# Kernel optimization log

Measured on AMD Instinct MI355X. Metric: run time of the kernel, lower is better.

The kernel has to match this reference:

```python
import jax, jax.numpy as jnp
import numpy as np

HIDDEN = 2560
HEADS = 32
HEAD_DIM = HIDDEN // HEADS  # 80
ROT = HEAD_DIM // 2         # partial_rotary_factor=0.5 -> 40
B = 2
S = 2048
T = B * S
THETA = 10000.0


def setup_inputs() -> dict:
    key = jax.random.key(0)
    k0, k1, k2, k3, k4 = jax.random.split(key, 5)
    hidden_states = jax.random.normal(k0, (T, HIDDEN), jnp.float32)
    w_qkv = jax.random.normal(k1, (3 * HIDDEN, HIDDEN), jnp.float32) * 0.02
    b_qkv = jax.random.normal(k2, (3 * HIDDEN,), jnp.float32) * 0.02
    w_o = jax.random.normal(k3, (HIDDEN, HIDDEN), jnp.float32) * 0.02
    b_o = jax.random.normal(k4, (HIDDEN,), jnp.float32) * 0.02
    # rotary tables for positions 0..S-1 per sequence, rotary_dim=ROT
    pos = jnp.tile(jnp.arange(S, dtype=jnp.float32), B)  # [T]
    inv_freq = 1.0 / (THETA ** (jnp.arange(0, ROT, 2, dtype=jnp.float32) / ROT))  # [ROT//2]
    freqs = pos[:, None] * inv_freq[None, :]  # [T, ROT//2]
    return {
        "hidden_states": hidden_states,
        "w_qkv": w_qkv,
        "b_qkv": b_qkv,
        "w_o": w_o,
        "b_o": b_o,
        "cos": jnp.cos(freqs),
        "sin": jnp.sin(freqs),
        "batch": B,
    }


def _apply_rope(x, cos, sin):
    # x: [T, H, D]; rotate first ROT dims NeoX-style (rotate_half)
    half = ROT // 2
    x1 = x[..., :half]
    x2 = x[..., half:ROT]
    c = cos[:, None, :]
    s = sin[:, None, :]
    return jnp.concatenate([x1 * c - x2 * s, x1 * s + x2 * c, x[..., ROT:]], axis=-1)


def reference(hidden_states, w_qkv, b_qkv, w_o, b_o, cos, sin, batch):
    t, hdim = hidden_states.shape
    seq = t // batch
    # fused QKV projection (with bias)
    qkv = hidden_states @ w_qkv.T + b_qkv  # [T, 3*HIDDEN]
    q, k, v = jnp.split(qkv, 3, axis=1)
    q = _apply_rope(q.reshape(t, HEADS, HEAD_DIM), cos, sin)
    k = _apply_rope(k.reshape(t, HEADS, HEAD_DIM), cos, sin)
    v = v.reshape(t, HEADS, HEAD_DIM)
    # prefill causal attention per sequence
    qb = q.reshape(batch, seq, HEADS, HEAD_DIM)
    kb = k.reshape(batch, seq, HEADS, HEAD_DIM)
    vb = v.reshape(batch, seq, HEADS, HEAD_DIM)
    scale = 1.0 / jnp.sqrt(jnp.float32(HEAD_DIM))
    scores = jnp.einsum("bqhd,bkhd->bhqk", qb, kb) * scale  # [B,H,S,S]
    causal = jnp.tril(jnp.ones((seq, seq), dtype=bool))
    scores = jnp.where(causal[None, None], scores, jnp.finfo(scores.dtype).min)
    attn = jax.nn.softmax(scores, axis=-1)
    out = jnp.einsum("bhqk,bkhd->bqhd", attn, vb).reshape(t, HIDDEN)
    return out @ w_o.T + b_o
```

## Files before the change

kernel.cpp:

```cpp
#include <hip/hip_runtime.h>
#include <hip/hip_bf16.h>

#define HID   2560
#define NH    32
#define HD    80
#define SEQ   2048
#define TTOT  4096
#define QKVN  7680

typedef float  f32x4  __attribute__((ext_vector_type(4)));
typedef short  short8 __attribute__((ext_vector_type(8)));
typedef __bf16 bf16x8 __attribute__((ext_vector_type(8)));
typedef __hip_bfloat16 bf16;

__device__ __forceinline__ float bf2f(bf16 h) { return __bfloat162float(h); }
__device__ __forceinline__ bf16  f2bf(float f) { return __float2bfloat16(f); }

__device__ __forceinline__ f32x4 mfma16(short8 a, short8 b, f32x4 c) {
  return __builtin_amdgcn_mfma_f32_16x16x32_bf16(
      __builtin_bit_cast(bf16x8, a), __builtin_bit_cast(bf16x8, b), c, 0, 0, 0);
}

typedef __attribute__((address_space(1))) const unsigned int as1_uint;
typedef __attribute__((address_space(3))) unsigned int       as3_uint;
__device__ __forceinline__ void gld16(const void* g, void* l) {
  __builtin_amdgcn_global_load_lds((as1_uint*)g, (as3_uint*)l, 16, 0, 0);
}

__global__ void detect_kernel(const unsigned short* __restrict__ hid, int* flag) {
  const int tid = threadIdx.x;
  const unsigned short u = hid[2 * (tid * 997)];
  const int e = (u >> 7) & 0xFF;
  const int sane = (u == 0 || (e >= 0x60 && e <= 0x8A)) ? 1 : 0;
  __shared__ int cnt;
  if (tid == 0) cnt = 0;
  __syncthreads();
  atomicAdd(&cnt, sane);
  __syncthreads();
  if (tid == 0) *flag = (cnt < 160) ? 1 : 0;
}

__global__ void convert_kernel(const void* __restrict__ src, bf16* __restrict__ dst,
                               int n8, const int* __restrict__ flag) {
  const bool isf32 = (*flag != 0);
  for (int i = blockIdx.x * 256 + threadIdx.x; i < n8; i += gridDim.x * 256) {
    if (isf32) {
      const float4* s = (const float4*)src;
      float4 a = s[2 * i], b = s[2 * i + 1];
      __align__(16) bf16 o8[8] = {f2bf(a.x), f2bf(a.y), f2bf(a.z), f2bf(a.w),
                                  f2bf(b.x), f2bf(b.y), f2bf(b.z), f2bf(b.w)};
      *(uint4*)(dst + 8 * i) = *(const uint4*)o8;
    } else {
      *(uint4*)(dst + 8 * i) = ((const uint4*)src)[i];
    }
  }
}

__global__ void emit_kernel(const bf16* __restrict__ src, void* __restrict__ dst,
                            int n8, const int* __restrict__ flag) {
  const bool isf32 = (*flag != 0);
  for (int i = blockIdx.x * 256 + threadIdx.x; i < n8; i += gridDim.x * 256) {
    uint4 v = *(const uint4*)(src + 8 * i);
    if (isf32) {
      const bf16* b = (const bf16*)&v;
      float4* d = (float4*)dst;
      d[2 * i]     = make_float4(bf2f(b[0]), bf2f(b[1]), bf2f(b[2]), bf2f(b[3]));
      d[2 * i + 1] = make_float4(bf2f(b[4]), bf2f(b[5]), bf2f(b[6]), bf2f(b[7]));
    } else {
      ((uint4*)dst)[i] = v;
    }
  }
}

__global__ __launch_bounds__(256) void gemm_bt_bias(
    const bf16* __restrict__ A, const bf16* __restrict__ B,
    const bf16* __restrict__ bias, bf16* __restrict__ C,
    int M, int N, int K)
{
  __shared__ __align__(16) bf16 lA[128 * 32];
  __shared__ __align__(16) bf16 lB[128 * 32];

  const int tid  = threadIdx.x;
  const int lane = tid & 63;
  const int wave = tid >> 6;
  const int quad = lane >> 4;
  const int l15  = lane & 15;
  const int m0 = blockIdx.x * 128;
  const int n0 = blockIdx.y * 128;
  const int wm = (wave & 1) * 64;
  const int wn = (wave >> 1) * 64;

  const int sr = tid >> 2;
  const int sc = (tid & 3) * 8;

  f32x4 acc[4][4];
  for (int i = 0; i < 4; i++)
    for (int j = 0; j < 4; j++) acc[i][j] = (f32x4)0.f;

  const bf16* Ap = A + (size_t)(m0 + sr) * K + sc;
  const bf16* Bp = B + (size_t)(n0 + sr) * K + sc;
  const size_t half = (size_t)64 * K;

  bf16* lA0 = lA + wave * 512;
  bf16* lA1 = lA + 2048 + wave * 512;
  bf16* lB0 = lB + wave * 512;
  bf16* lB1 = lB + 2048 + wave * 512;

  for (int k0 = 0; k0 < K; k0 += 32) {
    __syncthreads();
    gld16(Ap + k0,        lA0);
    gld16(Ap + half + k0, lA1);
    gld16(Bp + k0,        lB0);
    gld16(Bp + half + k0, lB1);
    __syncthreads();

    short8 af[4], bfr[4];
    for (int i = 0; i < 4; i++)
      af[i] = *(const short8*)&lA[(wm + i * 16 + l15) * 32 + quad * 8];
    for (int j = 0; j < 4; j++)
      bfr[j] = *(const short8*)&lB[(wn + j * 16 + l15) * 32 + quad * 8];
    for (int i = 0; i < 4; i++)
      for (int j = 0; j < 4; j++)
        acc[i][j] = mfma16(af[i], bfr[j], acc[i][j]);
  }

  for (int j = 0; j < 4; j++) {
    const int col = n0 + wn + j * 16 + l15;
    const float bv = bf2f(bias[col]);
    for (int i = 0; i < 4; i++) {
      const int rowb = m0 + wm + i * 16 + quad * 4;
      for (int r = 0; r < 4; r++)
        C[(size_t)(rowb + r) * N + col] = f2bf(acc[i][j][r] + bv);
    }
  }
}

__global__ __launch_bounds__(256) void rope_kernel(
    const bf16* __restrict__ qkv, const bf16* __restrict__ cosb,
    const bf16* __restrict__ sinb, bf16* __restrict__ Qr, bf16* __restrict__ Kr)
{
  const int t = blockIdx.x;
  const int b = t >> 11;
  const int s = t & 2047;
  const float qscale = 0.11180339887498949f;

  __shared__ float cs[20], sn[20];
  if (threadIdx.x < 20) cs[threadIdx.x] = bf2f(cosb[t * 20 + threadIdx.x]);
  if (threadIdx.x >= 32 && threadIdx.x < 52)
    sn[threadIdx.x - 32] = bf2f(sinb[t * 20 + (threadIdx.x - 32)]);
  __syncthreads();

  const bf16* qrow = qkv + (size_t)t * QKVN;
  const bf16* krow = qrow + HID;

  for (int idx = threadIdx.x; idx < HID; idx += 256) {
    const int h = idx / HD, d = idx % HD;
    const size_t off = ((size_t)(b * NH + h) * SEQ + s) * HD + d;
    float q, k;
    if (d < 20) {
      q = bf2f(qrow[h * HD + d]) * cs[d] - bf2f(qrow[h * HD + d + 20]) * sn[d];
      k = bf2f(krow[h * HD + d]) * cs[d] - bf2f(krow[h * HD + d + 20]) * sn[d];
    } else if (d < 40) {
      q = bf2f(qrow[h * HD + d - 20]) * sn[d - 20] + bf2f(qrow[h * HD + d]) * cs[d - 20];
      k = bf2f(krow[h * HD + d - 20]) * sn[d - 20] + bf2f(krow[h * HD + d]) * cs[d - 20];
    } else {
      q = bf2f(qrow[h * HD + d]);
      k = bf2f(krow[h * HD + d]);
    }
    Qr[off] = f2bf(q * qscale);
    Kr[off] = f2bf(k);
  }
}

__global__ __launch_bounds__(256) void vtrans_kernel(
    const bf16* __restrict__ qkv, bf16* __restrict__ Vt)
{
  const int bh = blockIdx.x;
  const int s0 = blockIdx.y * 64;
  const int b = bh >> 5, h = bh & 31;
  __shared__ bf16 tile[64][81];

  for (int e = threadIdx.x; e < 64 * HD; e += 256) {
    const int r = e / HD, d = e % HD;
    tile[r][d] = qkv[(size_t)(b * SEQ + s0 + r) * QKVN + 2 * HID + h * HD + d];
  }
  __syncthreads();
  for (int e = threadIdx.x; e < 64 * HD; e += 256) {
    const int d = e >> 6, r = e & 63;
    Vt[((size_t)bh * HD + d) * SEQ + s0 + r] = tile[r][d];
  }
}

__global__ __launch_bounds__(256, 3) void attn_kernel(
    const bf16* __restrict__ Qr, const bf16* __restrict__ Kr,
    const bf16* __restrict__ Vt, bf16* __restrict__ O)
{
  const int raw  = blockIdx.x;
  const int slot = raw >> 3;
  const int qblk = 15 - (slot & 15);
  const int bh   = ((slot >> 4) << 3) + (raw & 7);

  const int tid  = threadIdx.x;
  const int wave = tid >> 6;
  const int lane = tid & 63;
  const int quad = lane >> 4;
  const int l15  = lane & 15;
  const int qbase = qblk * 128;

  __shared__ __align__(16) bf16 stage[12544];
  __shared__ __align__(16) bf16 pt[4 * 2 * 1152];

  bf16* kt = stage;
  bf16* vt = stage + 5632;

  if (tid < 144) {
    const unsigned one2 = 0x3F803F80u;
    *(uint4*)&vt[5760 + tid * 8] = (uint4){one2, one2, one2, one2};
  }

  int goff[6];
#pragma unroll
  for (int it = 0; it < 6; it++) {
    const int j = tid + it * 256;
    if (j < 704) {
      const int r = j / 11; int c = j - 11 * r; if (c > 9) c = 0;
      goff[it] = r * 160 + c * 16;
    } else {
      const int j2 = j - 704;
      const int r = j2 / 9; int c = j2 - 9 * r; if (c > 7) c = 0;
      goff[it] = r * 4096 + c * 16;
    }
  }

  short8 aq[2][3];
#pragma unroll
  for (int f = 0; f < 2; f++) {
    const bf16* Qb = Qr + ((size_t)bh * SEQ + qbase + f * 64 + wave * 16 + l15) * HD + quad * 8;
    aq[f][0] = *(const short8*)(Qb);
    aq[f][1] = *(const short8*)(Qb + 32);
    aq[f][2] = *(const short8*)(Qb + 64);
    if (quad >= 2) aq[f][2] = (short8)0;
  }

  f32x4 o[2][6];
#pragma unroll
  for (int f = 0; f < 2; f++)
    for (int nt = 0; nt < 6; nt++) o[f][nt] = (f32x4)0.f;
  float m_i[2] = {-3e38f, -3e38f};

  const char* Kb8 = (const char*)(Kr + (size_t)bh * SEQ * HD);
  const char* Vb8 = (const char*)(Vt + (size_t)bh * HD * SEQ);
  const int nsteps = 2 * qblk + 2;
  const int rmax0 = qbase + wave * 16 + 15;

  for (int step = 0; step < nsteps; step++) {
    const int kvo = step * 64;
    const bool act0 = (kvo <= rmax0);

    __syncthreads();
    {
      const char* kb = Kb8 + kvo * 160;
      const char* vb = Vb8 + kvo * 2;
#pragma unroll
      for (int it = 0; it < 6; it++) {
        const int j = tid + it * 256;
        if (j < 1424) {
          bf16* ldsb = stage + (it * 256 + wave * 64) * 8;
          gld16((j < 704) ? (kb + goff[it]) : (vb + goff[it]), ldsb);
        }
      }
    }
    __syncthreads();

    f32x4 sv[2][4];
#pragma unroll
    for (int nt = 0; nt < 4; nt++) {
      const bf16* kr = &kt[(nt * 16 + l15) * 88 + quad * 8];
      short8 b0 = *(const short8*)(kr);
      short8 b1 = *(const short8*)(kr + 32);
      short8 b2 = *(const short8*)(kr + 64);
      if (act0) {
        f32x4 s = mfma16(b0, aq[0][0], (f32x4)0.f);
        s = mfma16(b1, aq[0][1], s);
        sv[0][nt] = mfma16(b2, aq[0][2], s);
      }
      f32x4 s1 = mfma16(b0, aq[1][0], (f32x4)0.f);
      s1 = mfma16(b1, aq[1][1], s1);
      sv[1][nt] = mfma16(b2, aq[1][2], s1);
    }

#pragma unroll
    for (int f = 0; f < 2; f++) {
      if (f == 0 && !act0) continue;
      const int mrel = qbase + f * 64 + wave * 16 - kvo;
      if (mrel < 63) {
        const int qrel = mrel + l15;
#pragma unroll
        for (int nt = 0; nt < 4; nt++) {
          f32x4 t = sv[f][nt];
#pragma unroll
          for (int r = 0; r < 4; r++)
            t[r] = (nt * 16 + quad * 4 + r <= qrel) ? t[r] : -3e38f;
          sv[f][nt] = t;
        }
      }
      float mx = fmaxf(fmaxf(sv[f][0][0], sv[f][0][1]), fmaxf(sv[f][0][2], sv[f][0][3]));
#pragma unroll
      for (int nt = 1; nt < 4; nt++)
        mx = fmaxf(mx, fmaxf(fmaxf(sv[f][nt][0], sv[f][nt][1]),
                             fmaxf(sv[f][nt][2], sv[f][nt][3])));
      mx = fmaxf(mx, __shfl_xor(mx, 16, 64));
      mx = fmaxf(mx, __shfl_xor(mx, 32, 64));
      const float mnew = fmaxf(m_i[f], mx);
      const float alpha = __expf(m_i[f] - mnew);
      m_i[f] = mnew;

      bf16* ptw = pt + (wave * 2 + f) * 1152;
#pragma unroll
      for (int nt = 0; nt < 4; nt++) {
        __align__(8) bf16 p4[4];
#pragma unroll
        for (int r = 0; r < 4; r++) p4[r] = f2bf(__expf(sv[f][nt][r] - mnew));
        *(unsigned long long*)&ptw[l15 * 72 + nt * 16 + quad * 4] =
            *(const unsigned long long*)p4;
      }
      float av[4];
#pragma unroll
      for (int r = 0; r < 4; r++) av[r] = __shfl(alpha, quad * 4 + r, 64);
#pragma unroll
      for (int nt = 0; nt < 6; nt++) {
        f32x4 t = o[f][nt];
        t[0] *= av[0]; t[1] *= av[1]; t[2] *= av[2]; t[3] *= av[3];
        o[f][nt] = t;
      }
    }

    asm volatile("s_waitcnt lgkmcnt(0)" ::: "memory");
    short8 pa00 = (short8)0, pa01 = (short8)0, pa10, pa11;
    {
      const bf16* p0 = pt + (wave * 2 + 0) * 1152 + l15 * 72 + quad * 8;
      const bf16* p1 = pt + (wave * 2 + 1) * 1152 + l15 * 72 + quad * 8;
      if (act0) { pa00 = *(const short8*)p0; pa01 = *(const short8*)(p0 + 32); }
      pa10 = *(const short8*)p1; pa11 = *(const short8*)(p1 + 32);
    }
#pragma unroll
    for (int nt = 0; nt < 6; nt++) {
      const bf16* vr = &vt[(nt * 16 + l15) * 72 + quad * 8];
      short8 v0 = *(const short8*)(vr);
      short8 v1 = *(const short8*)(vr + 32);
      if (act0) {
        o[0][nt] = mfma16(pa00, v0, o[0][nt]);
        o[0][nt] = mfma16(pa01, v1, o[0][nt]);
      }
      o[1][nt] = mfma16(pa10, v0, o[1][nt]);
      o[1][nt] = mfma16(pa11, v1, o[1][nt]);
    }
  }

  const int b = bh >> 5, h = bh & 31;
#pragma unroll
  for (int f = 0; f < 2; f++)
#pragma unroll
    for (int r = 0; r < 4; r++) {
      const float inv = 1.0f / o[f][5][r];
      const int trow = b * SEQ + qbase + f * 64 + wave * 16 + quad * 4 + r;
#pragma unroll
      for (int nt = 0; nt < 5; nt++)
        O[(size_t)trow * HID + h * HD + nt * 16 + l15] = f2bf(o[f][nt][r] * inv);
    }
}

extern "C" void kernel_launch(void* const* d_in, const int* in_sizes, int n_in,
                              void* d_out, int out_size, void* d_ws, size_t ws_size,
                              hipStream_t stream) {
  (void)in_sizes; (void)n_in; (void)ws_size;
  char* wsb = (char*)d_ws;

  int*  flag   = (int*) (wsb + 0);
  bf16* cos_c  = (bf16*)(wsb + 1024);
  bf16* sin_c  = (bf16*)(wsb + 165888);
  bf16* bqkv_c = (bf16*)(wsb + 329728);
  bf16* bo_c   = (bf16*)(wsb + 345088);
  bf16* wo_c   = (bf16*)(wsb + 1048576);
  bf16* qkv    = (bf16*)(wsb + 14155776);
  bf16* hid_c  = (bf16*)(wsb + 77070336);
  bf16* wqkv_c = (bf16*)(wsb + 98041856);
  bf16* Qr     = (bf16*)(wsb + 77070336);
  bf16* Kr     = (bf16*)(wsb + 98041856);
  bf16* Vt     = (bf16*)(wsb + 119013376);
  bf16* attn   = (bf16*)(wsb + 14155776);
  bf16* obuf   = (bf16*)(wsb + 35127296);

  detect_kernel<<<1, 256, 0, stream>>>((const unsigned short*)d_in[0], flag);
  convert_kernel<<<1024, 256, 0, stream>>>(d_in[0], hid_c,  TTOT * HID / 8, flag);
  convert_kernel<<<1024, 256, 0, stream>>>(d_in[1], wqkv_c, QKVN * HID / 8, flag);
  convert_kernel<<<4,    256, 0, stream>>>(d_in[2], bqkv_c, QKVN / 8,       flag);
  convert_kernel<<<1024, 256, 0, stream>>>(d_in[3], wo_c,   HID * HID / 8,  flag);
  convert_kernel<<<2,    256, 0, stream>>>(d_in[4], bo_c,   HID / 8,        flag);
  convert_kernel<<<40,   256, 0, stream>>>(d_in[5], cos_c,  TTOT * 20 / 8,  flag);
  convert_kernel<<<40,   256, 0, stream>>>(d_in[6], sin_c,  TTOT * 20 / 8,  flag);

  gemm_bt_bias<<<dim3(TTOT / 128, QKVN / 128), 256, 0, stream>>>(
      hid_c, wqkv_c, bqkv_c, qkv, TTOT, QKVN, HID);
  rope_kernel<<<dim3(TTOT), 256, 0, stream>>>(qkv, cos_c, sin_c, Qr, Kr);
  vtrans_kernel<<<dim3(64, SEQ / 64), 256, 0, stream>>>(qkv, Vt);
  attn_kernel<<<dim3(1024), 256, 0, stream>>>(Qr, Kr, Vt, attn);
  gemm_bt_bias<<<dim3(TTOT / 128, HID / 128), 256, 0, stream>>>(
      attn, wo_c, bo_c, obuf, TTOT, HID, HID);
  emit_kernel<<<1024, 256, 0, stream>>>(obuf, d_out, out_size / 8, flag);
}
```

Measured before the change: 647.9 us.

## Replace 128x128 GEMM with 256x256 double-buffered swizzled MFMA GEMM

```diff
diff --git a/kernel.cpp b/kernel.cpp
--- a/kernel.cpp
+++ b/kernel.cpp
@@ -72,65 +72,172 @@
   }
 }
 
-__global__ __launch_bounds__(256) void gemm_bt_bias(
+__global__ __launch_bounds__(512, 2) void gemm256_bias(
     const bf16* __restrict__ A, const bf16* __restrict__ B,
     const bf16* __restrict__ bias, bf16* __restrict__ C,
     int M, int N, int K)
 {
-  __shared__ __align__(16) bf16 lA[128 * 32];
-  __shared__ __align__(16) bf16 lB[128 * 32];
+  __shared__ __align__(16) bf16 lds[2][2][16384];
 
   const int tid  = threadIdx.x;
+  const int wid  = tid >> 6;
   const int lane = tid & 63;
-  const int wave = tid >> 6;
   const int quad = lane >> 4;
   const int l15  = lane & 15;
-  const int m0 = blockIdx.x * 128;
-  const int n0 = blockIdx.y * 128;
-  const int wm = (wave & 1) * 64;
-  const int wn = (wave >> 1) * 64;
-
-  const int sr = tid >> 2;
-  const int sc = (tid & 3) * 8;
-
-  f32x4 acc[4][4];
-  for (int i = 0; i < 4; i++)
-    for (int j = 0; j < 4; j++) acc[i][j] = (f32x4)0.f;
-
-  const bf16* Ap = A + (size_t)(m0 + sr) * K + sc;
-  const bf16* Bp = B + (size_t)(n0 + sr) * K + sc;
-  const size_t half = (size_t)64 * K;
-
-  bf16* lA0 = lA + wave * 512;
-  bf16* lA1 = lA + 2048 + wave * 512;
-  bf16* lB0 = lB + wave * 512;
-  bf16* lB1 = lB + 2048 + wave * 512;
-
-  for (int k0 = 0; k0 < K; k0 += 32) {
-    __syncthreads();
-    gld16(Ap + k0,        lA0);
-    gld16(Ap + half + k0, lA1);
-    gld16(Bp + k0,        lB0);
-    gld16(Bp + half + k0, lB1);
-    __syncthreads();
-
-    short8 af[4], bfr[4];
-    for (int i = 0; i < 4; i++)
-      af[i] = *(const short8*)&lA[(wm + i * 16 + l15) * 32 + quad * 8];
-    for (int j = 0; j < 4; j++)
-      bfr[j] = *(const short8*)&lB[(wn + j * 16 + l15) * 32 + quad * 8];
-    for (int i = 0; i < 4; i++)
-      for (int j = 0; j < 4; j++)
-        acc[i][j] = mfma16(af[i], bfr[j], acc[i][j]);
-  }
-
-  for (int j = 0; j < 4; j++) {
-    const int col = n0 + wn + j * 16 + l15;
-    const float bv = bf2f(bias[col]);
-    for (int i = 0; i < 4; i++) {
-      const int rowb = m0 + wm + i * 16 + quad * 4;
-      for (int r = 0; r < 4; r++)
-        C[(size_t)(rowb + r) * N + col] = f2bf(acc[i][j][r] + bv);
+  const int wr   = wid >> 2;
+  const int wc   = wid & 3;
+
+  int wgid;
+  {
+    const int nwg = gridDim.x;
+    const int q = nwg >> 3, r = nwg & 7;
+    const int xcd = blockIdx.x & 7, lin = blockIdx.x >> 3;
+    wgid = (xcd < r ? xcd * (q + 1) : r * (q + 1) + (xcd - r) * q) + lin;
+  }
+  const int gx = M >> 8;
+  const int m0 = (wgid % gx) << 8;
+  const int n0 = (wgid / gx) << 8;
+
+  const int NT = K >> 6;
+
+  const int rr   = tid >> 3;
+  const int cbyt = ((tid & 7) << 4) ^ ((rr & 7) << 4);
+  const size_t o1 = (size_t)rr * K + (cbyt >> 1);
+  const size_t o2 = o1 + (size_t)64 * K;
+
+  const bf16* Ab = A + (size_t)m0 * K;
+  const bf16* Bb = B + (size_t)n0 * K;
+
+#define STAGE(which, bufsel, half, tt)                                         \
+  {                                                                            \
+    const bf16* _s = ((which) ? Bb : Ab) + (size_t)(half) * 128 * K + (tt) * 64;\
+    bf16* _d = &lds[bufsel][which][(half) * 8192 + wid * 512];                 \
+    gld16(_s + o1, _d);                                                        \
+    gld16(_s + o2, _d + 4096);                                                 \
+  }
+
+  const int csw0 = ((quad ^ (l15 & 7)) << 4);
+  const int csw1 = (((4 | quad) ^ (l15 & 7)) << 4);
+
+  f32x4 acc[8][4];
+#pragma unroll
+  for (int i = 0; i < 8; ++i)
+#pragma unroll
+    for (int j = 0; j < 4; ++j) acc[i][j] = (f32x4)0.f;
+
+  short8 a[4][2], b[4][2];
+
+  STAGE(0, 0, 0, 0); STAGE(0, 0, 1, 0);
+  STAGE(1, 0, 0, 0); STAGE(1, 0, 1, 0);
+  STAGE(1, 1, 0, 1); STAGE(1, 1, 1, 1);
+  asm volatile("s_waitcnt vmcnt(4)" ::: "memory");
+  __builtin_amdgcn_s_barrier();
+
+  for (int t = 0; t < NT; ++t) {
+    const int cur = t & 1, nxt = cur ^ 1;
+    const bf16* Al = lds[cur][0];
+    const bf16* Bl = lds[cur][1];
+
+#pragma unroll
+    for (int mi = 0; mi < 4; ++mi) {
+      const char* p = (const char*)Al + (size_t)(wr * 128 + mi * 16 + l15) * 128;
+      a[mi][0] = *(const short8*)(p + csw0);
+      a[mi][1] = *(const short8*)(p + csw1);
+    }
+#pragma unroll
+    for (int n = 0; n < 2; ++n) {
+      const char* p = (const char*)Bl + (size_t)(wc * 64 + n * 16 + l15) * 128;
+      b[n][0] = *(const short8*)(p + csw0);
+      b[n][1] = *(const short8*)(p + csw1);
+    }
+    if (t + 1 < NT) STAGE(0, nxt, 0, t + 1);
+    __builtin_amdgcn_s_barrier();
+    asm volatile("s_waitcnt lgkmcnt(0)" ::: "memory");
+    __builtin_amdgcn_sched_barrier(0);
+    __builtin_amdgcn_s_setprio(1);
+#pragma unroll
+    for (int mi = 0; mi < 4; ++mi)
+#pragma unroll
+      for (int n = 0; n < 2; ++n) {
+        acc[mi][n] = mfma16(a[mi][0], b[n][0], acc[mi][n]);
+        acc[mi][n] = mfma16(a[mi][1], b[n][1], acc[mi][n]);
+      }
+    __builtin_amdgcn_s_setprio(0);
+    __builtin_amdgcn_s_barrier();
+
+#pragma unroll
+    for (int n = 2; n < 4; ++n) {
+      const char* p = (const char*)Bl + (size_t)(wc * 64 + n * 16 + l15) * 128;
+      b[n][0] = *(const short8*)(p + csw0);
+      b[n][1] = *(const short8*)(p + csw1);
+    }
+    if (t + 1 < NT) STAGE(0, nxt, 1, t + 1);
+    __builtin_amdgcn_s_barrier();
+    asm volatile("s_waitcnt lgkmcnt(0)" ::: "memory");
+    __builtin_amdgcn_sched_barrier(0);
+    __builtin_amdgcn_s_setprio(1);
+#pragma unroll
+    for (int mi = 0; mi < 4; ++mi)
+#pragma unroll
+      for (int n = 2; n < 4; ++n) {
+        acc[mi][n] = mfma16(a[mi][0], b[n][0], acc[mi][n]);
+        acc[mi][n] = mfma16(a[mi][1], b[n][1], acc[mi][n]);
+      }
+    __builtin_amdgcn_s_setprio(0);
+    __builtin_amdgcn_s_barrier();
+
+#pragma unroll
+    for (int mi = 0; mi < 4; ++mi) {
+      const char* p = (const char*)Al + (size_t)(wr * 128 + 64 + mi * 16 + l15) * 128;
+      a[mi][0] = *(const short8*)(p + csw0);
+      a[mi][1] = *(const short8*)(p + csw1);
+    }
+    if (t + 2 < NT) STAGE(1, cur, 0, t + 2);
+    __builtin_amdgcn_s_barrier();
+    asm volatile("s_waitcnt lgkmcnt(0)" ::: "memory");
+    __builtin_amdgcn_sched_barrier(0);
+    __builtin_amdgcn_s_setprio(1);
+#pragma unroll
+    for (int mi = 0; mi < 4; ++mi)
+#pragma unroll
+      for (int n = 2; n < 4; ++n) {
+        acc[4 + mi][n] = mfma16(a[mi][0], b[n][0], acc[4 + mi][n]);
+        acc[4 + mi][n] = mfma16(a[mi][1], b[n][1], acc[4 + mi][n]);
+      }
+    __builtin_amdgcn_s_setprio(0);
+    __builtin_amdgcn_s_barrier();
+
+    if (t + 2 < NT) STAGE(1, cur, 1, t + 2);
+    __builtin_amdgcn_s_barrier();
+    __builtin_amdgcn_s_setprio(1);
+#pragma unroll
+    for (int mi = 0; mi < 4; ++mi)
+#pragma unroll
+      for (int n = 0; n < 2; ++n) {
+        acc[4 + mi][n] = mfma16(a[mi][0], b[n][0], acc[4 + mi][n]);
+        acc[4 + mi][n] = mfma16(a[mi][1], b[n][1], acc[4 + mi][n]);
+      }
+    __builtin_amdgcn_s_setprio(0);
+    if (t + 2 < NT) {
+      asm volatile("s_waitcnt vmcnt(4)" ::: "memory");
+    } else if (t + 1 < NT) {
+      asm volatile("s_waitcnt vmcnt(0)" ::: "memory");
+    }
+    __builtin_amdgcn_s_barrier();
+  }
+#undef STAGE
+
+  const int crow = m0 + wr * 128 + quad * 4;
+  const int ccol = n0 + wc * 64 + l15;
+#pragma unroll
+  for (int n = 0; n < 4; ++n) {
+    const float bv = bf2f(bias[ccol + n * 16]);
+#pragma unroll
+    for (int mi = 0; mi < 8; ++mi) {
+      const int rb = crow + mi * 16;
+#pragma unroll
+      for (int r = 0; r < 4; ++r)
+        C[(size_t)(rb + r) * N + ccol + n * 16] = f2bf(acc[mi][n][r] + bv);
     }
   }
 }
@@ -400,12 +507,12 @@
   convert_kernel<<<40,   256, 0, stream>>>(d_in[5], cos_c,  TTOT * 20 / 8,  flag);
   convert_kernel<<<40,   256, 0, stream>>>(d_in[6], sin_c,  TTOT * 20 / 8,  flag);
 
-  gemm_bt_bias<<<dim3(TTOT / 128, QKVN / 128), 256, 0, stream>>>(
+  gemm256_bias<<<dim3((TTOT / 256) * (QKVN / 256)), 512, 0, stream>>>(
       hid_c, wqkv_c, bqkv_c, qkv, TTOT, QKVN, HID);
   rope_kernel<<<dim3(TTOT), 256, 0, stream>>>(qkv, cos_c, sin_c, Qr, Kr);
   vtrans_kernel<<<dim3(64, SEQ / 64), 256, 0, stream>>>(qkv, Vt);
   attn_kernel<<<dim3(1024), 256, 0, stream>>>(Qr, Kr, Vt, attn);
-  gemm_bt_bias<<<dim3(TTOT / 128, HID / 128), 256, 0, stream>>>(
+  gemm256_bias<<<dim3((TTOT / 256) * (HID / 256)), 512, 0, stream>>>(
       attn, wo_c, bo_c, obuf, TTOT, HID, HID);
   emit_kernel<<<1024, 256, 0, stream>>>(obuf, d_out, out_size / 8, flag);
 }
```

Result: faster. 600.8 us (-7.3%).
